# Kernel tuning notes

Hardware: AMD Instinct MI355X
Metric: run time of the kernel (lower is better)

The kernel has to match this reference:

```python
import jax, jax.numpy as jnp
import numpy as np

NEG_SLOPE = 0.2  # PyG GATConv default negative_slope
N_NODES = 50000


def gat_conv(x, src, dst, W, att_src, att_dst, bias, heads, out_ch):
    # x: [N, F_in]; src/dst: [E] (messages flow src -> dst, softmax over dst)
    N = x.shape[0]
    h = (x @ W).reshape(N, heads, out_ch)              # [N,H,C]
    a_src = jnp.sum(h * att_src, axis=-1)              # [N,H]
    a_dst = jnp.sum(h * att_dst, axis=-1)              # [N,H]
    e = jax.nn.leaky_relu(a_src[src] + a_dst[dst], NEG_SLOPE)   # [E,H]
    # numerically stable segment softmax over incoming edges of each dst node
    m = jax.ops.segment_max(e, dst, num_segments=N)    # [N,H]
    e = jnp.exp(e - m[dst])
    denom = jax.ops.segment_sum(e, dst, num_segments=N)
    alpha = e / (denom[dst] + 1e-16)                   # [E,H]
    msg = h[src] * alpha[:, :, None]                   # [E,H,C]
    out = jax.ops.segment_sum(msg, dst, num_segments=N)  # [N,H,C]
    return out.reshape(N, heads * out_ch) + bias


def add_self_loops(edge_index, num_nodes):
    loop = jnp.arange(num_nodes, dtype=edge_index.dtype)
    return jnp.concatenate([edge_index, jnp.stack([loop, loop])], axis=1)


def setup_inputs() -> dict:
    key = jax.random.key(0)
    ks = jax.random.split(key, 10)
    F_in, H, C, F_out = 256, 4, 64, 16
    x = jax.random.normal(ks[0], (N_NODES, F_in), dtype=jnp.float32)
    edge_index = jax.random.randint(ks[1], (2, 800000), 0, N_NODES, dtype=jnp.int64)
    s1 = 1.0 / np.sqrt(F_in)
    s2 = 1.0 / np.sqrt(H * C)
    return {
        "x": x,
        "edge_index": edge_index,
        "W1": jax.random.normal(ks[2], (F_in, H * C), dtype=jnp.float32) * s1,
        "att_src1": jax.random.normal(ks[3], (H, C), dtype=jnp.float32) * s2,
        "att_dst1": jax.random.normal(ks[4], (H, C), dtype=jnp.float32) * s2,
        "b1": jnp.zeros((H * C,), dtype=jnp.float32),
        "W2": jax.random.normal(ks[5], (H * C, F_out), dtype=jnp.float32) * s2,
        "att_src2": jax.random.normal(ks[6], (1, F_out), dtype=jnp.float32) * 0.25,
        "att_dst2": jax.random.normal(ks[7], (1, F_out), dtype=jnp.float32) * 0.25,
        "b2": jnp.zeros((F_out,), dtype=jnp.float32),
    }


def reference(x, edge_index, W1, att_src1, att_dst1, b1, W2, att_src2, att_dst2, b2):
    ei = add_self_loops(edge_index, x.shape[0])
    src, dst = ei[0], ei[1]
    H1, C1 = att_src1.shape
    h = gat_conv(x, src, dst, W1, att_src1, att_dst1, b1, H1, C1)
    h = jax.nn.relu(h)
    # F.dropout(training=False) is identity in eval mode
    H2, C2 = att_src2.shape
    out = gat_conv(h, src, dst, W2, att_src2, att_dst2, b2, H2, C2)
    return jax.nn.log_softmax(out, axis=1)
```

## Files before the change

kernel.cpp:

```cpp
#include <hip/hip_runtime.h>
#include <math.h>


typedef __attribute__((ext_vector_type(8))) short bf16x8;
typedef __attribute__((ext_vector_type(8))) unsigned short u16x8;
typedef __attribute__((ext_vector_type(4))) float f32x4;
typedef __attribute__((ext_vector_type(2))) float f32x2;

#define BCAP 1536

static __device__ inline unsigned short f2bf(float f) {
    unsigned u = __builtin_bit_cast(unsigned, f);
    unsigned r = (u + 0x7FFF + ((u >> 16) & 1)) >> 16;
    return (unsigned short)r;
}
static __device__ inline float bf2f(unsigned short u) {
    unsigned v = ((unsigned)u) << 16;
    return __builtin_bit_cast(float, v);
}
static __device__ inline float lrelu(float x) { return x > 0.f ? x : 0.2f * x; }

__global__ __launch_bounds__(256) void k_prep(const float* __restrict__ x,
                                              const float* __restrict__ W1,
                                              const float* __restrict__ b1,
                                              const float* __restrict__ W2,
                                              short* __restrict__ xb,
                                              unsigned short* __restrict__ csr,
                                              short* __restrict__ w1t,
                                              float* __restrict__ b1p,
                                              float* __restrict__ w2p,
                                              int* __restrict__ fill_bkt,
                                              float* __restrict__ a1s,
                                              float* __restrict__ a2s,
                                              unsigned* __restrict__ h1f8u,
                                              float* __restrict__ h2,
                                              int N, int nbuk) {
    long idx = (long)blockIdx.x * 256 + threadIdx.x;
    const long T = (long)N * 32;
    if (idx < T) {
        const float* xp = x + idx * 8;
        float4 f0 = *(const float4*)xp;
        float4 f1 = *(const float4*)(xp + 4);
        short b[8];
        b[0] = (short)f2bf(f0.x); b[1] = (short)f2bf(f0.y);
        b[2] = (short)f2bf(f0.z); b[3] = (short)f2bf(f0.w);
        b[4] = (short)f2bf(f1.x); b[5] = (short)f2bf(f1.y);
        b[6] = (short)f2bf(f1.z); b[7] = (short)f2bf(f1.w);
        *(bf16x8*)(xb + idx * 8) = *(bf16x8*)&b[0];
    }
    if (idx < (long)N * 16) {
        ushort4 v = make_ushort4((unsigned short)N, (unsigned short)N,
                                 (unsigned short)N, (unsigned short)N);
        if ((idx & 15) == 0) v.x = (unsigned short)(idx >> 4);
        *(ushort4*)(csr + idx * 4) = v;
    }
    if (idx < nbuk) fill_bkt[idx] = 0;
    if (idx < 256) {
        int ct = ((int)idx >> 6) * 64 + ((int)idx & 3) * 16 + (((int)idx & 63) >> 2);
        b1p[idx] = b1[ct];
    }
    if (idx < 4096) {
        int pp = (int)idx >> 4, c2 = (int)idx & 15;
        int ct = (pp >> 6) * 64 + (pp & 3) * 16 + ((pp & 63) >> 2);
        w2p[idx] = W2[ct * 16 + c2];
    }
    if (idx < 4) a1s[(long)N * 4 + idx] = -1e30f;
    if (idx == 4) a2s[N] = -1e30f;
    if (idx < 64) h1f8u[(long)N * 64 + idx] = 0u;
    if (idx < 16) h2[(long)N * 16 + idx] = 0.f;
    if (idx < 65536) {
        int n = (int)idx >> 8, k = (int)idx & 255;
        w1t[n * 256 + k] = (short)f2bf(W1[k * 256 + n]);
    }
}

__global__ __launch_bounds__(256) void k_bucketize(const int* __restrict__ ei,
                                                   int* __restrict__ fill_bkt,
                                                   unsigned* __restrict__ tmp,
                                                   int E0, int nbuk) {
    __shared__ int hist[1024];
    __shared__ int base[1024];
    const int t = threadIdx.x;
    const int e0 = blockIdx.x * 4096;
    for (int b = t; b < nbuk; b += 256) hist[b] = 0;
    __syncthreads();
    int ss[16], ds[16];
    int nm = 0;
#pragma unroll
    for (int k = 0; k < 16; ++k) {
        int e = e0 + t + k * 256;
        if (e < E0) {
            ss[nm] = ei[e];
            ds[nm] = ei[E0 + e];
            atomicAdd(&hist[ds[nm] >> 6], 1);
            ++nm;
        }
    }
    __syncthreads();
    for (int b = t; b < nbuk; b += 256) {
        int c = hist[b];
        base[b] = c ? atomicAdd(&fill_bkt[b], c) : 0;
        hist[b] = 0;
    }
    __syncthreads();
    for (int k = 0; k < nm; ++k) {
        int b = ds[k] >> 6;
        int r = base[b] + atomicAdd(&hist[b], 1);
        if (r < BCAP)
            tmp[(long)b * BCAP + r] = (unsigned)ss[k] | ((unsigned)(ds[k] & 63) << 16);
    }
}

__global__ __launch_bounds__(256) void k_csr_fill2(const unsigned* __restrict__ tmp,
                                                   const int* __restrict__ fill_bkt,
                                                   int* __restrict__ cnt,
                                                   unsigned short* __restrict__ csr,
                                                   int N, int nbuk) {
    __shared__ int lfill[64];
    const int b = blockIdx.x;
    const int t = threadIdx.x;
    if (t < 64) lfill[t] = 0;
    __syncthreads();
    int c = min(fill_bkt[b], BCAP);
    const unsigned* tp = tmp + (long)b * BCAP;
    for (int i = t; i < c; i += 256) {
        unsigned u = tp[i];
        int dl = u >> 16;
        int slot = atomicAdd(&lfill[dl], 1);
        if (slot < 63)
            csr[(((long)b * 64 + dl) << 6) + 1 + slot] = (unsigned short)(u & 0xffff);
    }
    __syncthreads();
    if (t < 64) {
        int d = b * 64 + t;
        if (d < N) cnt[d] = 1 + min(lfill[t], 63);
    }
}

__global__ __launch_bounds__(256) void k_gemm1_mfma(const short* __restrict__ Ab,
                                                    const short* __restrict__ Bt,
                                                    const float* __restrict__ att_s,
                                                    const float* __restrict__ att_d,
                                                    unsigned char* __restrict__ C8,
                                                    float* __restrict__ a1s,
                                                    float* __restrict__ a1d,
                                                    int M) {
    __shared__ short As[64][40];
    __shared__ short Bs[128][40];
    const int bm = blockIdx.y * 64;
    const int bn = blockIdx.x * 128;
    const int tid = threadIdx.x;
    const int lane = tid & 63;
    const int wave = tid >> 6;
    const int wm = (wave >> 1) * 32;
    const int wn = (wave & 1) * 64;
    const int l15 = lane & 15;
    const int l4 = lane >> 4;

    const int ar = tid >> 2, aq = (tid & 3) * 8;
    const int br = tid >> 1, bh = (tid & 1) * 16;

    f32x4 acc[2][4] = {};

    for (int k0 = 0; k0 < 256; k0 += 32) {
        {
            bf16x8 av;
            if (bm + ar < M) {
                av = *(const bf16x8*)&Ab[(long)(bm + ar) * 256 + k0 + aq];
            } else {
#pragma unroll
                for (int q = 0; q < 8; ++q) av[q] = 0;
            }
            *(bf16x8*)&As[ar][aq] = av;
            const short* p = &Bt[(long)(bn + br) * 256 + k0 + bh];
            *(bf16x8*)&Bs[br][bh] = *(const bf16x8*)p;
            *(bf16x8*)&Bs[br][bh + 8] = *(const bf16x8*)(p + 8);
        }
        __syncthreads();

        bf16x8 af[2], bfr[4];
#pragma unroll
        for (int i = 0; i < 2; ++i)
            af[i] = *(const bf16x8*)&As[wm + i * 16 + l15][l4 * 8];
#pragma unroll
        for (int j = 0; j < 4; ++j)
            bfr[j] = *(const bf16x8*)&Bs[wn + j * 16 + l15][l4 * 8];
#pragma unroll
        for (int i = 0; i < 2; ++i)
#pragma unroll
            for (int j = 0; j < 4; ++j)
                acc[i][j] = __builtin_amdgcn_mfma_f32_16x16x32_bf16(af[i], bfr[j], acc[i][j], 0, 0, 0);
        __syncthreads();
    }

    const int h = (bn + wn) >> 6;
    float aws[4], awd[4];
#pragma unroll
    for (int j = 0; j < 4; ++j) {
        aws[j] = att_s[h * 64 + j * 16 + l15];
        awd[j] = att_d[h * 64 + j * 16 + l15];
    }

#pragma unroll
    for (int i = 0; i < 2; ++i) {
#pragma unroll
        for (int r = 0; r < 4; ++r) {
            float sv = 0.f, dv = 0.f;
#pragma unroll
            for (int j = 0; j < 4; ++j) {
                sv += acc[i][j][r] * aws[j];
                dv += acc[i][j][r] * awd[j];
            }
#pragma unroll
            for (int o = 1; o < 16; o <<= 1) {
                sv += __shfl_xor(sv, o);
                dv += __shfl_xor(dv, o);
            }
            int row = bm + wm + i * 16 + l4 * 4 + r;
            if (row < M) {
                if (l15 == 0) { a1s[row * 4 + h] = sv; a1d[row * 4 + h] = dv; }
                int d = 0;
                d = __builtin_amdgcn_cvt_pk_fp8_f32(acc[i][0][r], acc[i][1][r], d, false);
                d = __builtin_amdgcn_cvt_pk_fp8_f32(acc[i][2][r], acc[i][3][r], d, true);
                *(unsigned*)&C8[(long)row * 256 + (bn + wn) + l15 * 4] = (unsigned)d;
            }
        }
    }
}

__global__ __launch_bounds__(256) void k_gather1(const unsigned char* __restrict__ h1f8,
                                                 const int* __restrict__ cnt,
                                                 const unsigned short* __restrict__ csr,
                                                 const float* __restrict__ as1,
                                                 const float* __restrict__ ad1,
                                                 const float* __restrict__ b1p,
                                                 unsigned short* __restrict__ out1b,
                                                 int N) {
    int wid = blockIdx.x * 4 + (threadIdx.x >> 6);
    int lane = threadIdx.x & 63;
    if (wid >= N) return;

    const int es = lane >> 4;
    const int cl = lane & 15;
    const int hc = cl >> 2;
    const float adh = ad1[wid * 4 + hc];

    int c = min(cnt[wid], 64);
    int len4 = (c + 3) & ~3;
    const unsigned short* seg = csr + ((long)wid << 6);
    const char* as1c = (const char*)as1 + hc * 4;
    const char* h1c  = (const char*)h1f8 + cl * 16;

    float dacc = 0.f;
    f32x2 acc2[8] = {};
#pragma unroll 2
    for (int j0 = 0; j0 < len4; j0 += 4) {
        int sv = seg[j0 + es];
        float a = __expf(lrelu(*(const float*)(as1c + ((long)sv << 4)) + adh));
        dacc += a;
        f32x2 av = {a, a};
        uint4 v = *(const uint4*)(h1c + ((long)sv << 8));
        unsigned w[4] = {v.x, v.y, v.z, v.w};
#pragma unroll
        for (int q = 0; q < 4; ++q) {
            f32x2 lo = __builtin_amdgcn_cvt_pk_f32_fp8((int)w[q], false);
            f32x2 hi = __builtin_amdgcn_cvt_pk_f32_fp8((int)w[q], true);
            acc2[q * 2 + 0] += av * lo;
            acc2[q * 2 + 1] += av * hi;
        }
    }
    dacc += __shfl_xor(dacc, 16);
    dacc += __shfl_xor(dacc, 32);
    const float inv_c = 1.f / (dacc + 1e-16f);

    float accf[16];
#pragma unroll
    for (int q = 0; q < 8; ++q) { accf[2 * q] = acc2[q].x; accf[2 * q + 1] = acc2[q].y; }
#pragma unroll
    for (int q = 0; q < 16; ++q) {
        accf[q] += __shfl_xor(accf[q], 16);
        accf[q] += __shfl_xor(accf[q], 32);
    }
    if (lane < 16) {
        unsigned pk[8];
#pragma unroll
        for (int q = 0; q < 8; ++q) {
            float v0 = fmaxf(accf[q * 2 + 0] * inv_c + b1p[cl * 16 + q * 2 + 0], 0.f);
            float v1 = fmaxf(accf[q * 2 + 1] * inv_c + b1p[cl * 16 + q * 2 + 1], 0.f);
            pk[q] = (unsigned)f2bf(v0) | ((unsigned)f2bf(v1) << 16);
        }
        unsigned short* dst = &out1b[(long)wid * 256 + cl * 16];
        *(uint4*)dst = make_uint4(pk[0], pk[1], pk[2], pk[3]);
        *(uint4*)(dst + 8) = make_uint4(pk[4], pk[5], pk[6], pk[7]);
    }
}

__global__ __launch_bounds__(256) void k_gemm2(const unsigned short* __restrict__ Xb,
                                               const float* __restrict__ Wp,
                                               const float* __restrict__ att_s,
                                               const float* __restrict__ att_d,
                                               float* __restrict__ h2,
                                               float* __restrict__ a2s,
                                               float* __restrict__ a2d, int N) {
    __shared__ float Ws[256 * 16];
    for (int i = threadIdx.x; i < 1024; i += 256)
        ((float4*)Ws)[i] = ((const float4*)Wp)[i];
    __syncthreads();
    int r = threadIdx.x >> 4, c = threadIdx.x & 15;
    int row = blockIdx.x * 16 + r;
    if (row >= N) return;
    const unsigned short* xr = Xb + (long)row * 256;
    float acc = 0.f;
    for (int k = 0; k < 256; k += 8) {
        u16x8 xv = *(const u16x8*)&xr[k];
#pragma unroll
        for (int q = 0; q < 8; ++q)
            acc += bf2f(xv[q]) * Ws[(k + q) * 16 + c];
    }
    h2[row * 16 + c] = acc;
    float vs = acc * att_s[c];
    float vd = acc * att_d[c];
    for (int o = 1; o < 16; o <<= 1) { vs += __shfl_xor(vs, o); vd += __shfl_xor(vd, o); }
    if (c == 0) { a2s[row] = vs; a2d[row] = vd; }
}

__global__ __launch_bounds__(256) void k_gather2(const float* __restrict__ h2,
                                                 const int* __restrict__ cnt,
                                                 const unsigned short* __restrict__ csr,
                                                 const float* __restrict__ a2s,
                                                 const float* __restrict__ a2d,
                                                 const float* __restrict__ b2,
                                                 float* __restrict__ out, int N) {
    int wid = blockIdx.x * 4 + (threadIdx.x >> 6);
    int lane = threadIdx.x & 63;
    if (wid >= N) return;
    float adh = a2d[wid];
    const int es = lane >> 4;
    const int c = lane & 15;

    int cc = min(cnt[wid], 64);
    int len4 = (cc + 3) & ~3;
    const unsigned short* seg = csr + ((long)wid << 6);
    const char* a2c = (const char*)a2s;
    const char* h2c = (const char*)h2 + c * 4;

    float dacc = 0.f;
    float acc = 0.f;
#pragma unroll 2
    for (int j0 = 0; j0 < len4; j0 += 4) {
        int sv = seg[j0 + es];
        float a = __expf(lrelu(*(const float*)(a2c + ((long)sv << 2)) + adh));
        dacc += a;
        acc += a * *(const float*)(h2c + ((long)sv << 6));
    }
    acc += __shfl_xor(acc, 16);
    acc += __shfl_xor(acc, 32);
    dacc += __shfl_xor(dacc, 16);
    dacc += __shfl_xor(dacc, 32);
    float inv = 1.f / (dacc + 1e-16f);
    float v = acc * inv + b2[c];
    float mx = v;
    for (int o = 1; o < 16; o <<= 1) mx = fmaxf(mx, __shfl_xor(mx, o));
    float se = __expf(v - mx);
    for (int o = 1; o < 16; o <<= 1) se += __shfl_xor(se, o);
    float r = v - mx - logf(se);
    if (lane < 16) out[(long)wid * 16 + c] = r;
}

extern "C" void kernel_launch(void* const* d_in, const int* in_sizes, int n_in,
                              void* d_out, int out_size, void* d_ws, size_t ws_size,
                              hipStream_t stream) {
    const float* x    = (const float*)d_in[0];
    const int*   ei   = (const int*)d_in[1];
    const float* W1   = (const float*)d_in[2];
    const float* as1w = (const float*)d_in[3];
    const float* ad1w = (const float*)d_in[4];
    const float* b1   = (const float*)d_in[5];
    const float* W2   = (const float*)d_in[6];
    const float* as2w = (const float*)d_in[7];
    const float* ad2w = (const float*)d_in[8];
    const float* b2   = (const float*)d_in[9];
    float* out = (float*)d_out;

    const int N    = in_sizes[0] / 256;
    const int E0   = in_sizes[1] / 2;
    const int NBUK = (N + 63) >> 6;

    char* p = (char*)d_ws;
    unsigned char*  h1f8  = (unsigned char*)p;  p += (size_t)(N + 1) * 256;
    unsigned short* out1b = (unsigned short*)p; p += (size_t)N * 256 * sizeof(short);
    float* h2     = (float*)p; p += (size_t)(N + 1) * 16 * sizeof(float);
    float* a1s    = (float*)p; p += (size_t)(N + 1) * 4 * sizeof(float);
    float* a1d    = (float*)p; p += (size_t)N * 4 * sizeof(float);
    float* a2s    = (float*)p; p += (size_t)(N + 1) * sizeof(float);
    float* a2d    = (float*)p; p += (size_t)N * sizeof(float);
    float* b1p    = (float*)p; p += (size_t)256 * sizeof(float);
    float* w2p    = (float*)p; p += (size_t)4096 * sizeof(float);
    int*   cnt    = (int*)p;   p += (size_t)N * sizeof(int);
    int*   fillbk = (int*)p;   p += (size_t)NBUK * sizeof(int);
    short* w1t    = (short*)p; p += (size_t)256 * 256 * sizeof(short);
    unsigned short* csr = (unsigned short*)p; p += (size_t)N * 64 * sizeof(unsigned short);
    unsigned* tmp = (unsigned*)p; p += (size_t)NBUK * BCAP * sizeof(unsigned);

    short* xb = (short*)out1b;

    const int NW = (N + 3) / 4;

    const long T = (long)N * 32;
    hipLaunchKernelGGL(k_prep, dim3((unsigned)((T + 255) / 256)), dim3(256), 0, stream,
                       x, W1, b1, W2, xb, csr, w1t, b1p, w2p, fillbk, a1s, a2s,
                       (unsigned*)h1f8, h2, N, NBUK);

    hipLaunchKernelGGL(k_bucketize, dim3((E0 + 4095) / 4096), dim3(256), 0, stream,
                       ei, fillbk, tmp, E0, NBUK);
    hipLaunchKernelGGL(k_csr_fill2, dim3(NBUK), dim3(256), 0, stream,
                       tmp, fillbk, cnt, csr, N, NBUK);

    hipLaunchKernelGGL(k_gemm1_mfma, dim3(2, (N + 63) / 64), dim3(256), 0, stream,
                       xb, w1t, as1w, ad1w, h1f8, a1s, a1d, N);
    hipLaunchKernelGGL(k_gather1, dim3(NW), dim3(256), 0, stream,
                       h1f8, cnt, csr, a1s, a1d, b1p, out1b, N);

    hipLaunchKernelGGL(k_gemm2, dim3((N + 15) / 16), dim3(256), 0, stream,
                       out1b, w2p, as2w, ad2w, h2, a2s, a2d, N);
    hipLaunchKernelGGL(k_gather2, dim3(NW), dim3(256), 0, stream,
                       h2, cnt, csr, a2s, a2d, b2, out, N);
}
```

Before: 232.9 us.

## Merge CSR fill into GEMM1 launch and vectorize layer-2 gather

The CSR fill kernel and the first MFMA GEMM become one launch whose leading blocks do the bucket fill and whose remaining blocks do the GEMM tiles. The two are independent, so they can run concurrently and one launch and its gap go away. The layer-2 gather now has each lane handle 4 channels through float4 loads, so 16 edges are processed per step instead of 4, which shortens the loop and cuts the number of index loads. The fused kernel keeps the GEMM's shared-memory footprint in the fill blocks, and the gather now pads each segment to a multiple of 16.

```diff
diff --git a/kernel.cpp b/kernel.cpp
--- a/kernel.cpp
+++ b/kernel.cpp
@@ -111,44 +111,49 @@
     }
 }
 
-__global__ __launch_bounds__(256) void k_csr_fill2(const unsigned* __restrict__ tmp,
-                                                   const int* __restrict__ fill_bkt,
-                                                   int* __restrict__ cnt,
-                                                   unsigned short* __restrict__ csr,
-                                                   int N, int nbuk) {
-    __shared__ int lfill[64];
-    const int b = blockIdx.x;
-    const int t = threadIdx.x;
-    if (t < 64) lfill[t] = 0;
-    __syncthreads();
-    int c = min(fill_bkt[b], BCAP);
-    const unsigned* tp = tmp + (long)b * BCAP;
-    for (int i = t; i < c; i += 256) {
-        unsigned u = tp[i];
-        int dl = u >> 16;
-        int slot = atomicAdd(&lfill[dl], 1);
-        if (slot < 63)
-            csr[(((long)b * 64 + dl) << 6) + 1 + slot] = (unsigned short)(u & 0xffff);
-    }
-    __syncthreads();
-    if (t < 64) {
-        int d = b * 64 + t;
-        if (d < N) cnt[d] = 1 + min(lfill[t], 63);
-    }
-}
-
-__global__ __launch_bounds__(256) void k_gemm1_mfma(const short* __restrict__ Ab,
-                                                    const short* __restrict__ Bt,
-                                                    const float* __restrict__ att_s,
-                                                    const float* __restrict__ att_d,
-                                                    unsigned char* __restrict__ C8,
-                                                    float* __restrict__ a1s,
-                                                    float* __restrict__ a1d,
-                                                    int M) {
+__global__ __launch_bounds__(256) void k_gemm1_fill(
+        const short* __restrict__ Ab,
+        const short* __restrict__ Bt,
+        const float* __restrict__ att_s,
+        const float* __restrict__ att_d,
+        unsigned char* __restrict__ C8,
+        float* __restrict__ a1s,
+        float* __restrict__ a1d,
+        int M,
+        const unsigned* __restrict__ tmp,
+        const int* __restrict__ fill_bkt,
+        int* __restrict__ cnt,
+        unsigned short* __restrict__ csr,
+        int N, int nbuk) {
     __shared__ short As[64][40];
     __shared__ short Bs[128][40];
-    const int bm = blockIdx.y * 64;
-    const int bn = blockIdx.x * 128;
+    __shared__ int lfill[64];
+
+    if ((int)blockIdx.x < nbuk) {
+        const int b = blockIdx.x;
+        const int t = threadIdx.x;
+        if (t < 64) lfill[t] = 0;
+        __syncthreads();
+        int c = min(fill_bkt[b], BCAP);
+        const unsigned* tp = tmp + (long)b * BCAP;
+        for (int i = t; i < c; i += 256) {
+            unsigned u = tp[i];
+            int dl = u >> 16;
+            int slot = atomicAdd(&lfill[dl], 1);
+            if (slot < 63)
+                csr[(((long)b * 64 + dl) << 6) + 1 + slot] = (unsigned short)(u & 0xffff);
+        }
+        __syncthreads();
+        if (t < 64) {
+            int d = b * 64 + t;
+            if (d < N) cnt[d] = 1 + min(lfill[t], 63);
+        }
+        return;
+    }
+
+    const int g = (int)blockIdx.x - nbuk;
+    const int bm = (g >> 1) * 64;
+    const int bn = (g & 1) * 128;
     const int tid = threadIdx.x;
     const int lane = tid & 63;
     const int wave = tid >> 6;
@@ -335,36 +340,42 @@
     int lane = threadIdx.x & 63;
     if (wid >= N) return;
     float adh = a2d[wid];
-    const int es = lane >> 4;
-    const int c = lane & 15;
+    const int es = lane >> 2;
+    const int c4 = (lane & 3) << 2;
 
     int cc = min(cnt[wid], 64);
-    int len4 = (cc + 3) & ~3;
+    int len16 = (cc + 15) & ~15;
     const unsigned short* seg = csr + ((long)wid << 6);
-    const char* a2c = (const char*)a2s;
-    const char* h2c = (const char*)h2 + c * 4;
 
     float dacc = 0.f;
-    float acc = 0.f;
-#pragma unroll 2
-    for (int j0 = 0; j0 < len4; j0 += 4) {
+    float a0 = 0.f, a1 = 0.f, a2 = 0.f, a3 = 0.f;
+    for (int j0 = 0; j0 < len16; j0 += 16) {
         int sv = seg[j0 + es];
-        float a = __expf(lrelu(*(const float*)(a2c + ((long)sv << 2)) + adh));
+        float a = __expf(lrelu(a2s[sv] + adh));
         dacc += a;
-        acc += a * *(const float*)(h2c + ((long)sv << 6));
-    }
-    acc += __shfl_xor(acc, 16);
-    acc += __shfl_xor(acc, 32);
-    dacc += __shfl_xor(dacc, 16);
-    dacc += __shfl_xor(dacc, 32);
+        float4 hv = *(const float4*)&h2[((long)sv << 4) + c4];
+        a0 += a * hv.x; a1 += a * hv.y; a2 += a * hv.z; a3 += a * hv.w;
+    }
+#pragma unroll
+    for (int o = 4; o < 64; o <<= 1) {
+        a0 += __shfl_xor(a0, o); a1 += __shfl_xor(a1, o);
+        a2 += __shfl_xor(a2, o); a3 += __shfl_xor(a3, o);
+        dacc += __shfl_xor(dacc, o);
+    }
     float inv = 1.f / (dacc + 1e-16f);
-    float v = acc * inv + b2[c];
-    float mx = v;
-    for (int o = 1; o < 16; o <<= 1) mx = fmaxf(mx, __shfl_xor(mx, o));
-    float se = __expf(v - mx);
-    for (int o = 1; o < 16; o <<= 1) se += __shfl_xor(se, o);
-    float r = v - mx - logf(se);
-    if (lane < 16) out[(long)wid * 16 + c] = r;
+    float v0 = a0 * inv + b2[c4 + 0];
+    float v1 = a1 * inv + b2[c4 + 1];
+    float v2 = a2 * inv + b2[c4 + 2];
+    float v3 = a3 * inv + b2[c4 + 3];
+    float mx = fmaxf(fmaxf(v0, v1), fmaxf(v2, v3));
+    mx = fmaxf(mx, __shfl_xor(mx, 1));
+    mx = fmaxf(mx, __shfl_xor(mx, 2));
+    float se = __expf(v0 - mx) + __expf(v1 - mx) + __expf(v2 - mx) + __expf(v3 - mx);
+    se += __shfl_xor(se, 1);
+    se += __shfl_xor(se, 2);
+    float ls = mx + logf(se);
+    if (lane < 4)
+        *(float4*)&out[(long)wid * 16 + c4] = make_float4(v0 - ls, v1 - ls, v2 - ls, v3 - ls);
 }
 
 extern "C" void kernel_launch(void* const* d_in, const int* in_sizes, int n_in,
@@ -413,11 +424,12 @@
 
     hipLaunchKernelGGL(k_bucketize, dim3((E0 + 4095) / 4096), dim3(256), 0, stream,
                        ei, fillbk, tmp, E0, NBUK);
-    hipLaunchKernelGGL(k_csr_fill2, dim3(NBUK), dim3(256), 0, stream,
+
+    const int GB = 2 * ((N + 63) / 64);
+    hipLaunchKernelGGL(k_gemm1_fill, dim3(NBUK + GB), dim3(256), 0, stream,
+                       xb, w1t, as1w, ad1w, h1f8, a1s, a1d, N,
                        tmp, fillbk, cnt, csr, N, NBUK);
 
-    hipLaunchKernelGGL(k_gemm1_mfma, dim3(2, (N + 63) / 64), dim3(256), 0, stream,
-                       xb, w1t, as1w, ad1w, h1f8, a1s, a1d, N);
     hipLaunchKernelGGL(k_gather1, dim3(NW), dim3(256), 0, stream,
                        h1f8, cnt, csr, a1s, a1d, b1p, out1b, N);
 
```

Result: no change. 229.4 us (median of 2 runs) (-1.5%).
